# Kernel tuning notes

Hardware: AMD Instinct MI355X
Metric: run time of the kernel (lower is better)

Reference implementation:

```python
import jax, jax.numpy as jnp
import numpy as np

HIDDEN = 4096
NUM_HEADS = 32
HEAD_DIM = HIDDEN // NUM_HEADS
BATCH = 2
SEQ = 2048


def setup_inputs() -> dict:
    key = jax.random.key(0)
    k0, k1, k2, k3 = jax.random.split(key, 4)
    hidden_states = jax.random.normal(k0, (BATCH, SEQ, HIDDEN), dtype=jnp.float32)
    scale = 1.0 / np.sqrt(HIDDEN)
    # torch nn.Linear weight shape: [out_features, in_features]
    wq = jax.random.normal(k1, (HIDDEN, HIDDEN), dtype=jnp.float32) * scale
    wk = jax.random.normal(k2, (HIDDEN, HIDDEN), dtype=jnp.float32) * scale
    wv = jax.random.normal(k3, (HIDDEN, HIDDEN), dtype=jnp.float32) * scale
    return {"hidden_states": hidden_states, "wq": wq, "wk": wk, "wv": wv}


def reference(hidden_states, wq, wk, wv):
    b, s, _ = hidden_states.shape
    # torch Linear: y = x @ W.T
    q = hidden_states @ wq.T
    k = hidden_states @ wk.T
    v = hidden_states @ wv.T
    # [b, s, h, d] -> [b, h, s, d]
    q = q.reshape(b, s, NUM_HEADS, HEAD_DIM).transpose(0, 2, 1, 3)
    k = k.reshape(b, s, NUM_HEADS, HEAD_DIM).transpose(0, 2, 1, 3)
    v = v.reshape(b, s, NUM_HEADS, HEAD_DIM).transpose(0, 2, 1, 3)
    attn_weights = jnp.einsum('bhqd,bhkd->bhqk', q, k) / np.sqrt(HEAD_DIM)
    attn_weights = jax.nn.softmax(attn_weights, axis=-1)
    out = jnp.einsum('bhqk,bhkd->bhqd', attn_weights, v)
    out = out.transpose(0, 2, 1, 3).reshape(b, s, HIDDEN)
    return (out, attn_weights)
```

## Files before the change

### kernel.cpp

```cpp
#include <hip/hip_runtime.h>

typedef __attribute__((ext_vector_type(8))) short short8v;
typedef __attribute__((ext_vector_type(4))) float f32x4;
typedef __attribute__((ext_vector_type(16))) float f32x16;

#define HID 4096
#define SEQL 2048
#define NH 32
#define HD 128
#define MROWS 4096


__device__ __forceinline__ void gl_lds16(const void* g, void* l) {
  __builtin_amdgcn_global_load_lds(
      (const __attribute__((address_space(1))) unsigned int*)g,
      (__attribute__((address_space(3))) unsigned int*)l, 16, 0, 0);
}

__device__ __forceinline__ unsigned short f2bf(float x) {
  union { float f; unsigned u; } v; v.f = x;
  return (unsigned short)((v.u + 0x7FFFu + ((v.u >> 16) & 1u)) >> 16);
}

#define BAR()    __builtin_amdgcn_s_barrier()
#define LGKM0()  asm volatile("s_waitcnt lgkmcnt(0)" ::: "memory")
#define VM4()    asm volatile("s_waitcnt vmcnt(4)" ::: "memory")
#define SCHED0() __builtin_amdgcn_sched_barrier(0)


__global__ __launch_bounds__(256) void cast_bf16_kernel(
    const float* __restrict__ s0, const float* __restrict__ s1,
    const float* __restrict__ s2, const float* __restrict__ s3,
    unsigned short* __restrict__ dst)
{
  const float* src = blockIdx.y == 0 ? s0 : blockIdx.y == 1 ? s1
                   : blockIdx.y == 2 ? s2 : s3;
  unsigned short* d = dst + (size_t)blockIdx.y * ((size_t)HID * MROWS);
  size_t i = (size_t)blockIdx.x * blockDim.x + threadIdx.x;
  const float4* s4 = (const float4*)src;
  float4 a = s4[2 * i], b = s4[2 * i + 1];
  short8v o;
  o[0] = (short)f2bf(a.x); o[1] = (short)f2bf(a.y);
  o[2] = (short)f2bf(a.z); o[3] = (short)f2bf(a.w);
  o[4] = (short)f2bf(b.x); o[5] = (short)f2bf(b.y);
  o[6] = (short)f2bf(b.z); o[7] = (short)f2bf(b.w);
  *(short8v*)(d + i * 8) = o;
}

__global__ __launch_bounds__(512, 2) void gemm_qkv_kernel(
    const unsigned short* __restrict__ A,
    const unsigned short* __restrict__ Wq,
    const unsigned short* __restrict__ Wk,
    const unsigned short* __restrict__ Wv,
    unsigned short* __restrict__ Qo,
    unsigned short* __restrict__ Ko,
    unsigned short* __restrict__ Vo)
{
  __shared__ unsigned short As[2 * 256 * 64];
  __shared__ unsigned short Bs[2 * 256 * 64];
  const int bid = blockIdx.x;
  const int swz = (bid & 7) * 96 + (bid >> 3);
  const int which = swz >> 8;
  const int id = swz & 255;
  const unsigned short* W = which == 0 ? Wq : which == 1 ? Wk : Wv;
  unsigned short* C = which == 0 ? Qo : which == 1 ? Ko : Vo;

  const int t = threadIdx.x;
  const int lane = t & 63;
  const int w = t >> 6;
  const int wr = w >> 2, wc = w & 3;
  const int bm = (id >> 4) << 8;
  const int bn = (id & 15) << 8;

  const int srow = t >> 3;
  const int sslot = t & 7;
  const int scol = (sslot ^ (srow & 7)) << 3;
  const size_t arow0 = (size_t)(bm + srow) * HID;
  const size_t brow0 = (size_t)(bn + srow) * HID;
  const int ldsoff = (t & ~63) << 4;

#define STAGE(isB, tile, half) do {                                          \
    int _k = ((tile) & 63) << 6;                                             \
    const unsigned short* _s = (isB) ? W : A;                                \
    size_t _r = ((isB) ? brow0 : arow0) + (size_t)(half) * 128 * HID;        \
    char* _d = (char*)((isB) ? Bs : As) + ((tile) & 1) * 32768 +             \
               (half) * 16384 + ldsoff;                                      \
    gl_lds16(&_s[_r + _k + scol], _d);                                       \
    gl_lds16(&_s[_r + (size_t)64 * HID + _k + scol], _d + 8192);             \
  } while (0)

  short8v av[4][2];
  short8v bv[2][4];
  f32x4 acc[8][4] = {};

#define RD_A(d, mbase)                                                        \
  _Pragma("unroll") for (int mm = 0; mm < 4; ++mm) {                          \
    int row = wr * 128 + ((mbase) + mm) * 16 + (lane & 15);                   \
    av[mm][0] = *(const short8v*)&As[(d)*16384 + row*64 + ((   (lane>>4)) ^ (row&7))*8]; \
    av[mm][1] = *(const short8v*)&As[(d)*16384 + row*64 + ((4+ (lane>>4)) ^ (row&7))*8]; \
  }
#define RD_B(d, kk)                                                           \
  _Pragma("unroll") for (int nn = 0; nn < 4; ++nn) {                          \
    int row = wc * 64 + nn * 16 + (lane & 15);                                \
    bv[kk][nn] = *(const short8v*)&Bs[(d)*16384 + row*64 + (((kk)*4 + (lane>>4)) ^ (row&7))*8]; \
  }
#define MFMA16(mbase, kk)                                                     \
  __builtin_amdgcn_s_setprio(1);                                              \
  _Pragma("unroll") for (int mm = 0; mm < 4; ++mm)                            \
  _Pragma("unroll") for (int nn = 0; nn < 4; ++nn)                            \
    acc[(mbase)+mm][nn] = __builtin_amdgcn_mfma_f32_16x16x32_bf16(            \
        av[mm][kk], bv[kk][nn], acc[(mbase)+mm][nn], 0, 0, 0);                \
  __builtin_amdgcn_s_setprio(0);

  STAGE(1, 0, 0); STAGE(1, 0, 1); STAGE(0, 0, 0); STAGE(0, 0, 1);
  STAGE(1, 1, 0); STAGE(1, 1, 1);
  VM4(); BAR(); SCHED0();

  for (int i = 0; i < 32; ++i) {
    int j = 2 * i;
    RD_A(0, 0); RD_B(0, 0); STAGE(0, j + 1, 0);
    BAR(); LGKM0(); SCHED0(); MFMA16(0, 0); BAR(); SCHED0();
    RD_B(0, 1); STAGE(0, j + 1, 1);
    BAR(); LGKM0(); SCHED0(); MFMA16(0, 1); BAR(); SCHED0();
    RD_A(0, 4); STAGE(1, j + 2, 0);
    BAR(); LGKM0(); SCHED0(); MFMA16(4, 0); BAR(); SCHED0();
    STAGE(0, j + 2, 0); VM4();
    BAR(); MFMA16(4, 1); BAR(); SCHED0();
    RD_A(1, 0); RD_B(1, 0); STAGE(1, j + 2, 1);
    BAR(); LGKM0(); SCHED0(); MFMA16(0, 0); BAR(); SCHED0();
    RD_B(1, 1); STAGE(0, j + 2, 1);
    BAR(); LGKM0(); SCHED0(); MFMA16(0, 1); BAR(); SCHED0();
    RD_A(1, 4); STAGE(1, j + 3, 0);
    BAR(); LGKM0(); SCHED0(); MFMA16(4, 0); BAR(); SCHED0();
    STAGE(1, j + 3, 1); VM4();
    BAR(); MFMA16(4, 1); BAR(); SCHED0();
  }

#pragma unroll
  for (int m = 0; m < 8; ++m) {
#pragma unroll
    for (int n = 0; n < 4; ++n) {
      int r0 = bm + wr * 128 + m * 16 + (lane >> 4) * 4;
      int col = bn + wc * 64 + n * 16 + (lane & 15);
      if (which < 2) {
#pragma unroll
        for (int j = 0; j < 4; ++j)
          C[(size_t)(r0 + j) * HID + col] = f2bf(acc[m][n][j]);
      } else {
        int head = col >> 7, dd = col & 127;
        int bb = r0 >> 11, s = r0 & 2047;
        unsigned short* p = C + ((size_t)(bb * NH + head) * HD + dd) * (size_t)SEQL + s;
        union { unsigned short us[4]; uint2 v; } pk;
        pk.us[0] = f2bf(acc[m][n][0]); pk.us[1] = f2bf(acc[m][n][1]);
        pk.us[2] = f2bf(acc[m][n][2]); pk.us[3] = f2bf(acc[m][n][3]);
        *(uint2*)p = pk.v;
      }
    }
  }
#undef STAGE
#undef RD_A
#undef RD_B
#undef MFMA16
}

__global__ __launch_bounds__(256) void attn_kernel(
    const unsigned short* __restrict__ Q,
    const unsigned short* __restrict__ K,
    const unsigned short* __restrict__ Vt,
    float* __restrict__ attn_out,
    float* __restrict__ out)
{
  const int flat = blockIdx.x;
  const int sw = (flat & 7) * 128 + (flat >> 3);
  const int q0 = (sw & 15) << 7;
  const int bh = sw >> 4;
  const int b = bh >> 5, h = bh & 31;
  const int t = threadIdx.x, lane = t & 63, w = t >> 6;
  const int l31 = lane & 31, g = lane >> 5;
  const float a = 0.08838834764831845f * 1.4426950408889634f;

  __shared__ unsigned short Ks[2 * 64 * 128];
  __shared__ unsigned short Vs[2 * 128 * 64];
  __shared__ unsigned short Ps[4][32 * 64];

  short8v qf[8];
  {
    const unsigned short* qrow =
        Q + (size_t)(b * SEQL + q0 + w * 32 + l31) * HID + h * HD + g * 8;
#pragma unroll
    for (int c = 0; c < 8; ++c) qf[c] = *(const short8v*)(qrow + c * 16);
  }

  const int krow_s = t >> 4;
  const int kchunk_s = t & 15;
  const int vrow_s = t >> 3;
  const int vchunk_s = t & 7;

  float lsum[16];
#pragma unroll
  for (int r = 0; r < 16; ++r) lsum[r] = 0.f;

  {
#pragma unroll
    for (int i = 0; i < 4; ++i) {
      int krow = i * 16 + krow_s;
      int kchunk = kchunk_s ^ (krow & 15);
      gl_lds16(&K[(size_t)(b * SEQL + krow) * HID + h * HD + kchunk * 8],
               (char*)Ks + i * 4096 + w * 1024);
    }
  }
  __syncthreads();
  int buf = 0;
  for (int kt = 0; kt < SEQL; kt += 64) {
    if (kt + 64 < SEQL) {
#pragma unroll
      for (int i = 0; i < 4; ++i) {
        int krow = i * 16 + krow_s;
        int kchunk = kchunk_s ^ (krow & 15);
        gl_lds16(&K[(size_t)(b * SEQL + kt + 64 + krow) * HID + h * HD + kchunk * 8],
                 (char*)Ks + (buf ^ 1) * 16384 + i * 4096 + w * 1024);
      }
    }
    const unsigned short* Kc = Ks + buf * 8192;
    f32x16 s0 = {}, s1 = {};
    __builtin_amdgcn_s_setprio(1);
#pragma unroll
    for (int c = 0; c < 8; ++c) {
      int r0 = l31;
      short8v k0v = *(const short8v*)&Kc[r0 * 128 + (((c * 2 + g) ^ (r0 & 15)) * 8)];
      int r1 = 32 + l31;
      short8v k1v = *(const short8v*)&Kc[r1 * 128 + (((c * 2 + g) ^ (r1 & 15)) * 8)];
      s0 = __builtin_amdgcn_mfma_f32_32x32x16_bf16(qf[c], k0v, s0, 0, 0, 0);
      s1 = __builtin_amdgcn_mfma_f32_32x32x16_bf16(qf[c], k1v, s1, 0, 0, 0);
    }
    __builtin_amdgcn_s_setprio(0);
#pragma unroll
    for (int r = 0; r < 16; ++r)
      lsum[r] += exp2f(s0[r] * a) + exp2f(s1[r] * a);
    __syncthreads();
    buf ^= 1;
  }

  float lb[16];
#pragma unroll
  for (int r = 0; r < 16; ++r) {
    float e = lsum[r];
#pragma unroll
    for (int d = 1; d < 32; d <<= 1) e += __shfl_xor(e, d);
    lb[r] = -__log2f(e);
  }

  f32x16 o[4] = {};
  float* abase = attn_out + ((size_t)bh * SEQL + q0 + w * 32) * (size_t)SEQL + l31;

  {
#pragma unroll
    for (int i = 0; i < 4; ++i) {
      int krow = i * 16 + krow_s;
      int kchunk = kchunk_s ^ (krow & 15);
      gl_lds16(&K[(size_t)(b * SEQL + krow) * HID + h * HD + kchunk * 8],
               (char*)Ks + i * 4096 + w * 1024);
      int vrow = i * 32 + vrow_s;
      int vchunk = vchunk_s ^ (vrow & 7);
      gl_lds16(&Vt[((size_t)bh * HD + vrow) * (size_t)SEQL + vchunk * 8],
               (char*)Vs + i * 4096 + w * 1024);
    }
  }
  __syncthreads();
  buf = 0;
  for (int kt = 0; kt < SEQL; kt += 64) {
    if (kt + 64 < SEQL) {
#pragma unroll
      for (int i = 0; i < 4; ++i) {
        int krow = i * 16 + krow_s;
        int kchunk = kchunk_s ^ (krow & 15);
        gl_lds16(&K[(size_t)(b * SEQL + kt + 64 + krow) * HID + h * HD + kchunk * 8],
                 (char*)Ks + (buf ^ 1) * 16384 + i * 4096 + w * 1024);
        int vrow = i * 32 + vrow_s;
        int vchunk = vchunk_s ^ (vrow & 7);
        gl_lds16(&Vt[((size_t)bh * HD + vrow) * (size_t)SEQL + kt + 64 + vchunk * 8],
                 (char*)Vs + (buf ^ 1) * 16384 + i * 4096 + w * 1024);
      }
    }
    const unsigned short* Kc = Ks + buf * 8192;
    const unsigned short* Vc = Vs + buf * 8192;
    f32x16 s0 = {}, s1 = {};
    __builtin_amdgcn_s_setprio(1);
#pragma unroll
    for (int c = 0; c < 8; ++c) {
      int r0 = l31;
      short8v k0v = *(const short8v*)&Kc[r0 * 128 + (((c * 2 + g) ^ (r0 & 15)) * 8)];
      int r1 = 32 + l31;
      short8v k1v = *(const short8v*)&Kc[r1 * 128 + (((c * 2 + g) ^ (r1 & 15)) * 8)];
      s0 = __builtin_amdgcn_mfma_f32_32x32x16_bf16(qf[c], k0v, s0, 0, 0, 0);
      s1 = __builtin_amdgcn_mfma_f32_32x32x16_bf16(qf[c], k1v, s1, 0, 0, 0);
    }
    __builtin_amdgcn_s_setprio(0);
#pragma unroll
    for (int r = 0; r < 16; ++r) {
      int qr = (r & 3) + ((r >> 2) << 3) + g * 4;
      float p0 = exp2f(__builtin_fmaf(s0[r], a, lb[r]));
      float p1 = exp2f(__builtin_fmaf(s1[r], a, lb[r]));
      __builtin_nontemporal_store(p0, &abase[(size_t)qr * SEQL + kt]);
      __builtin_nontemporal_store(p1, &abase[(size_t)qr * SEQL + kt + 32]);
      int sl0 = ((l31 >> 3)) ^ (qr & 7);
      int sl1 = (4 + (l31 >> 3)) ^ (qr & 7);
      Ps[w][qr * 64 + sl0 * 8 + (l31 & 7)] = f2bf(p0);
      Ps[w][qr * 64 + sl1 * 8 + (l31 & 7)] = f2bf(p1);
    }
    __builtin_amdgcn_s_setprio(1);
#pragma unroll
    for (int c2 = 0; c2 < 4; ++c2) {
      short8v pa = *(const short8v*)&Ps[w][l31 * 64 + (((c2 * 2 + g) ^ (l31 & 7)) * 8)];
#pragma unroll
      for (int n = 0; n < 4; ++n) {
        int vrow = n * 32 + l31;
        short8v vb = *(const short8v*)&Vc[vrow * 64 + (((c2 * 2 + g) ^ (vrow & 7)) * 8)];
        o[n] = __builtin_amdgcn_mfma_f32_32x32x16_bf16(pa, vb, o[n], 0, 0, 0);
      }
    }
    __builtin_amdgcn_s_setprio(0);
    __syncthreads();
    buf ^= 1;
  }

  float* obase = out + (size_t)(b * SEQL + q0 + w * 32) * HID + h * HD + l31;
#pragma unroll
  for (int n = 0; n < 4; ++n)
#pragma unroll
    for (int r = 0; r < 16; ++r) {
      int qr = (r & 3) + ((r >> 2) << 3) + g * 4;
      __builtin_nontemporal_store(o[n][r], &obase[(size_t)qr * HID + n * 32]);
    }
}


extern "C" void kernel_launch(void* const* d_in, const int* in_sizes, int n_in,
                              void* d_out, int out_size, void* d_ws, size_t ws_size,
                              hipStream_t stream) {
  const float* X  = (const float*)d_in[0];
  const float* wq = (const float*)d_in[1];
  const float* wk = (const float*)d_in[2];
  const float* wv = (const float*)d_in[3];

  const size_t NEL = (size_t)HID * MROWS;
  unsigned short* ws  = (unsigned short*)d_ws;
  unsigned short* Xb  = ws;
  unsigned short* Wqb = ws + NEL;
  unsigned short* Wkb = ws + 2 * NEL;
  unsigned short* Wvb = ws + 3 * NEL;
  unsigned short* Qb  = ws + 4 * NEL;
  unsigned short* Kb  = ws + 5 * NEL;
  unsigned short* Vtb = ws + 6 * NEL;

  float* outp  = (float*)d_out;
  float* attnp = outp + NEL;

  cast_bf16_kernel<<<dim3(8192, 4), 256, 0, stream>>>(X, wq, wk, wv, Xb);
  gemm_qkv_kernel<<<768, 512, 0, stream>>>(Xb, Wqb, Wkb, Wvb, Qb, Kb, Vtb);
  attn_kernel<<<1024, 256, 0, stream>>>(Qb, Kb, Vtb, attnp, outp);
}
```

Measured before the change: 789.1 us.

## Use 512-thread attention blocks with triple-buffered K/V and explicit vmcnt waits

The attention kernel now uses 8 waves per block, each block covering 256 query rows, so every staged K/V tile feeds twice as many rows. The K/V shared-memory staging goes from double to triple buffering, with a prefetch distance of two tiles. Full __syncthreads are replaced by explicit vmcnt waits plus a raw barrier, aiming to keep global-to-LDS loads in flight across iterations. The trade-off is more LDS per block (about 128KB) and fewer blocks, which may cut occupancy and expose some tail imbalance.

```diff
diff --git a/kernel.cpp b/kernel.cpp
--- a/kernel.cpp
+++ b/kernel.cpp
@@ -24,6 +24,8 @@
 
 #define BAR()    __builtin_amdgcn_s_barrier()
 #define LGKM0()  asm volatile("s_waitcnt lgkmcnt(0)" ::: "memory")
+#define VM0()    asm volatile("s_waitcnt vmcnt(0)" ::: "memory")
+#define VM2()    asm volatile("s_waitcnt vmcnt(2)" ::: "memory")
 #define VM4()    asm volatile("s_waitcnt vmcnt(4)" ::: "memory")
 #define SCHED0() __builtin_amdgcn_sched_barrier(0)
 
@@ -163,7 +165,7 @@
 #undef MFMA16
 }
 
-__global__ __launch_bounds__(256) void attn_kernel(
+__global__ __launch_bounds__(512, 2) void attn_kernel(
     const unsigned short* __restrict__ Q,
     const unsigned short* __restrict__ K,
     const unsigned short* __restrict__ Vt,
@@ -171,17 +173,17 @@
     float* __restrict__ out)
 {
   const int flat = blockIdx.x;
-  const int sw = (flat & 7) * 128 + (flat >> 3);
-  const int q0 = (sw & 15) << 7;
-  const int bh = sw >> 4;
+  const int sw = (flat & 7) * 64 + (flat >> 3);
+  const int bh = sw >> 3;
+  const int q0 = (sw & 7) << 8;
   const int b = bh >> 5, h = bh & 31;
   const int t = threadIdx.x, lane = t & 63, w = t >> 6;
   const int l31 = lane & 31, g = lane >> 5;
   const float a = 0.08838834764831845f * 1.4426950408889634f;
 
-  __shared__ unsigned short Ks[2 * 64 * 128];
-  __shared__ unsigned short Vs[2 * 128 * 64];
-  __shared__ unsigned short Ps[4][32 * 64];
+  __shared__ unsigned short Ks[3 * 64 * 128];
+  __shared__ unsigned short Vs[3 * 128 * 64];
+  __shared__ unsigned short Ps[8][32 * 64];
 
   short8v qf[8];
   {
@@ -191,37 +193,37 @@
     for (int c = 0; c < 8; ++c) qf[c] = *(const short8v*)(qrow + c * 16);
   }
 
-  const int krow_s = t >> 4;
-  const int kchunk_s = t & 15;
-  const int vrow_s = t >> 3;
-  const int vchunk_s = t & 7;
+  const int kc = (w << 6) + lane;
+  const int krow0 = kc >> 4, kslot = kc & 15;
+  const int vrow0 = kc >> 3, vslot = kc & 7;
+  const unsigned short* Ksrc =
+      K + (size_t)(b * SEQL + krow0) * HID + h * HD + ((kslot ^ (krow0 & 15)) << 3);
+  const unsigned short* Vsrc =
+      Vt + ((size_t)bh * HD + vrow0) * (size_t)SEQL + ((vslot ^ (vrow0 & 7)) << 3);
+  const int ldsw = w << 10;
+
+#define STAGE_K(tile, buf) do {                                              \
+    const unsigned short* _k = Ksrc + (size_t)((tile) * 64) * HID;           \
+    char* _d = (char*)Ks + (buf) * 16384 + ldsw;                             \
+    gl_lds16(_k, _d);                                                        \
+    gl_lds16(_k + (size_t)32 * HID, _d + 8192);                              \
+  } while (0)
+#define STAGE_V(tile, buf) do {                                              \
+    const unsigned short* _v = Vsrc + (tile) * 64;                           \
+    char* _d = (char*)Vs + (buf) * 16384 + ldsw;                             \
+    gl_lds16(_v, _d);                                                        \
+    gl_lds16(_v + (size_t)64 * SEQL, _d + 8192);                             \
+  } while (0)
 
   float lsum[16];
 #pragma unroll
   for (int r = 0; r < 16; ++r) lsum[r] = 0.f;
 
-  {
-#pragma unroll
-    for (int i = 0; i < 4; ++i) {
-      int krow = i * 16 + krow_s;
-      int kchunk = kchunk_s ^ (krow & 15);
-      gl_lds16(&K[(size_t)(b * SEQL + krow) * HID + h * HD + kchunk * 8],
-               (char*)Ks + i * 4096 + w * 1024);
-    }
-  }
-  __syncthreads();
-  int buf = 0;
-  for (int kt = 0; kt < SEQL; kt += 64) {
-    if (kt + 64 < SEQL) {
-#pragma unroll
-      for (int i = 0; i < 4; ++i) {
-        int krow = i * 16 + krow_s;
-        int kchunk = kchunk_s ^ (krow & 15);
-        gl_lds16(&K[(size_t)(b * SEQL + kt + 64 + krow) * HID + h * HD + kchunk * 8],
-                 (char*)Ks + (buf ^ 1) * 16384 + i * 4096 + w * 1024);
-      }
-    }
-    const unsigned short* Kc = Ks + buf * 8192;
+  STAGE_K(0, 0); STAGE_K(1, 1);
+  VM2(); BAR();
+  for (int i = 0; i < 32; ++i) {
+    if (i < 30) STAGE_K(i + 2, (i + 2) % 3);
+    const unsigned short* Kc = Ks + (i % 3) * 8192;
     f32x16 s0 = {}, s1 = {};
     __builtin_amdgcn_s_setprio(1);
 #pragma unroll
@@ -237,8 +239,8 @@
 #pragma unroll
     for (int r = 0; r < 16; ++r)
       lsum[r] += exp2f(s0[r] * a) + exp2f(s1[r] * a);
-    __syncthreads();
-    buf ^= 1;
+    if (i < 30) { VM2(); } else if (i == 30) { VM0(); }
+    BAR();
   }
 
   float lb[16];
@@ -253,37 +255,13 @@
   f32x16 o[4] = {};
   float* abase = attn_out + ((size_t)bh * SEQL + q0 + w * 32) * (size_t)SEQL + l31;
 
-  {
-#pragma unroll
-    for (int i = 0; i < 4; ++i) {
-      int krow = i * 16 + krow_s;
-      int kchunk = kchunk_s ^ (krow & 15);
-      gl_lds16(&K[(size_t)(b * SEQL + krow) * HID + h * HD + kchunk * 8],
-               (char*)Ks + i * 4096 + w * 1024);
-      int vrow = i * 32 + vrow_s;
-      int vchunk = vchunk_s ^ (vrow & 7);
-      gl_lds16(&Vt[((size_t)bh * HD + vrow) * (size_t)SEQL + vchunk * 8],
-               (char*)Vs + i * 4096 + w * 1024);
-    }
-  }
-  __syncthreads();
-  buf = 0;
-  for (int kt = 0; kt < SEQL; kt += 64) {
-    if (kt + 64 < SEQL) {
-#pragma unroll
-      for (int i = 0; i < 4; ++i) {
-        int krow = i * 16 + krow_s;
-        int kchunk = kchunk_s ^ (krow & 15);
-        gl_lds16(&K[(size_t)(b * SEQL + kt + 64 + krow) * HID + h * HD + kchunk * 8],
-                 (char*)Ks + (buf ^ 1) * 16384 + i * 4096 + w * 1024);
-        int vrow = i * 32 + vrow_s;
-        int vchunk = vchunk_s ^ (vrow & 7);
-        gl_lds16(&Vt[((size_t)bh * HD + vrow) * (size_t)SEQL + kt + 64 + vchunk * 8],
-                 (char*)Vs + (buf ^ 1) * 16384 + i * 4096 + w * 1024);
-      }
-    }
-    const unsigned short* Kc = Ks + buf * 8192;
-    const unsigned short* Vc = Vs + buf * 8192;
+  STAGE_K(0, 0); STAGE_V(0, 0); STAGE_K(1, 1); STAGE_V(1, 1);
+  VM4(); BAR();
+  for (int i = 0; i < 32; ++i) {
+    if (i < 30) { STAGE_K(i + 2, (i + 2) % 3); STAGE_V(i + 2, (i + 2) % 3); }
+    const unsigned short* Kc = Ks + (i % 3) * 8192;
+    const unsigned short* Vc = Vs + (i % 3) * 8192;
+    const int kt = i * 64;
     f32x16 s0 = {}, s1 = {};
     __builtin_amdgcn_s_setprio(1);
 #pragma unroll
@@ -320,8 +298,8 @@
       }
     }
     __builtin_amdgcn_s_setprio(0);
-    __syncthreads();
-    buf ^= 1;
+    if (i < 30) { VM4(); } else if (i == 30) { VM0(); }
+    BAR();
   }
 
   float* obase = out + (size_t)(b * SEQL + q0 + w * 32) * HID + h * HD + l31;
@@ -332,6 +310,8 @@
       int qr = (r & 3) + ((r >> 2) << 3) + g * 4;
       __builtin_nontemporal_store(o[n][r], &obase[(size_t)qr * HID + n * 32]);
     }
+#undef STAGE_K
+#undef STAGE_V
 }
 
 
@@ -358,5 +338,5 @@
 
   cast_bf16_kernel<<<dim3(8192, 4), 256, 0, stream>>>(X, wq, wk, wv, Xb);
   gemm_qkv_kernel<<<768, 512, 0, stream>>>(Xb, Wqb, Wkb, Wvb, Qb, Kb, Vtb);
-  attn_kernel<<<1024, 256, 0, stream>>>(Qb, Kb, Vtb, attnp, outp);
-}
+  attn_kernel<<<512, 512, 0, stream>>>(Qb, Kb, Vtb, attnp, outp);
+}
```

Result: no change. 785.7 us, median of 3 (-0.4%).
